# Performance work log

Hardware: AMD Instinct MI355X
Metric: run time of the kernel (lower is better)

## Reference

```python
import jax, jax.numpy as jnp
import numpy as np

N_HEADS = 6
HEAD_SIZE = 64


def setup_inputs() -> dict:
    key = jax.random.key(0)
    k1, k2, k3, k4 = jax.random.split(key, 4)
    B, T, C = 8, 2048, N_HEADS * HEAD_SIZE
    x = jax.random.normal(k1, (B, T, C), dtype=jnp.float32)
    # small init scale keeps softmax logits in a sane range
    w_qkv = jax.random.normal(k2, (C, 3 * C), dtype=jnp.float32) * 0.05
    w_proj = jax.random.normal(k3, (C, C), dtype=jnp.float32) * 0.05
    b_proj = jax.random.normal(k4, (C,), dtype=jnp.float32) * 0.05
    return {"x": x, "w_qkv": w_qkv, "w_proj": w_proj, "b_proj": b_proj}


def reference(x, w_qkv, w_proj, b_proj):
    B, T, C = x.shape
    qkv = x @ w_qkv                      # [B, T, 3C]
    q, k, v = jnp.split(qkv, 3, axis=2)
    # [B, T, C] -> [B, H, T, D]
    def heads(t):
        return t.reshape(B, T, N_HEADS, HEAD_SIZE).transpose(0, 2, 1, 3)
    q, k, v = heads(q), heads(k), heads(v)
    scale = HEAD_SIZE ** -0.5
    scores = jnp.einsum('bhqd,bhkd->bhqk', q, k) * scale   # [B, H, T, T]
    causal = jnp.tril(jnp.ones((T, T), dtype=bool))
    scores = jnp.where(causal[None, None], scores, jnp.float32(-jnp.inf))
    weights = jax.nn.softmax(scores, axis=-1)
    # dropout is identity in eval mode
    out = jnp.einsum('bhqk,bhkd->bhqd', weights, v)          # [B, H, T, D]
    out = out.transpose(0, 2, 1, 3).reshape(B, T, C)
    return out @ w_proj + b_proj
```

## Files before the change

kernel.cpp:

```cpp
#include <hip/hip_runtime.h>
#include <hip/hip_bf16.h>

typedef __bf16 bf16_t;
typedef __bf16 bf16x8 __attribute__((ext_vector_type(8)));
typedef __bf16 bf16x4 __attribute__((ext_vector_type(4)));
typedef float floatx4 __attribute__((ext_vector_type(4)));
typedef unsigned uint32x2 __attribute__((ext_vector_type(2)));

#define MFMA16(a, b, c) __builtin_amdgcn_mfma_f32_16x16x32_bf16(a, b, c, 0, 0, 0)

#if __has_builtin(__builtin_amdgcn_exp2f)
#define EXP2F(x) __builtin_amdgcn_exp2f(x)
#else
#define EXP2F(x) __expf((x)*0.693147180559945f)
#endif

__device__ __forceinline__ void async_copy16(const bf16_t* g, bf16_t* l) {
    __builtin_amdgcn_global_load_lds((const __attribute__((address_space(1))) void*)g,
                                     (__attribute__((address_space(3))) void*)l, 16, 0, 0);
}

__device__ __forceinline__ unsigned cvt_pk_bf16(float lo, float hi) {
    unsigned r;
    asm("v_cvt_pk_bf16_f32 %0, %1, %2" : "=v"(r) : "v"(lo), "v"(hi));
    return r;
}

__device__ __forceinline__ void plane32(unsigned& x, unsigned& y) {
#if __has_builtin(__builtin_amdgcn_permlane32_swap)
    uint32x2 r = __builtin_amdgcn_permlane32_swap(x, y, false, false);
    x = r[0]; y = r[1];
#else
    asm("v_permlane32_swap_b32 %0, %1" : "+v"(x), "+v"(y));
#endif
}
__device__ __forceinline__ void plane16(unsigned& x, unsigned& y) {
#if __has_builtin(__builtin_amdgcn_permlane16_swap)
    uint32x2 r = __builtin_amdgcn_permlane16_swap(x, y, false, false);
    x = r[0]; y = r[1];
#else
    asm("v_permlane16_swap_b32 %0, %1" : "+v"(x), "+v"(y));
#endif
}

__device__ __forceinline__ bf16x8 pack_pfrag(const floatx4& sE, const floatx4& sO) {
    unsigned a0 = cvt_pk_bf16(sE[0], sE[1]);
    unsigned a1 = cvt_pk_bf16(sE[2], sE[3]);
    unsigned b0 = cvt_pk_bf16(sO[0], sO[1]);
    unsigned b1 = cvt_pk_bf16(sO[2], sO[3]);
    plane32(a0, b0);
    plane32(a1, b1);
    plane16(a0, b0);
    plane16(a1, b1);
    union { unsigned u[4]; bf16x8 v; } r;
    r.u[0] = a0; r.u[1] = a1; r.u[2] = b0; r.u[3] = b1;
    return r.v;
}

__global__ void prep_fused(const float* __restrict__ x, const float* __restrict__ w_qkv,
                           const float* __restrict__ w_proj, bf16_t* __restrict__ xb,
                           bf16_t* __restrict__ wqkvT, bf16_t* __restrict__ wprojT) {
    const int bx = blockIdx.x, tid = threadIdx.x;
    if (bx < 3072) {
        size_t i = ((size_t)bx * 256 + tid) * 8;
        float4 v0 = *(const float4*)(x + i);
        float4 v1 = *(const float4*)(x + i + 4);
        bf16x8 o = {(bf16_t)v0.x, (bf16_t)v0.y, (bf16_t)v0.z, (bf16_t)v0.w,
                    (bf16_t)v1.x, (bf16_t)v1.y, (bf16_t)v1.z, (bf16_t)v1.w};
        *(bf16x8*)(xb + i) = o;
        return;
    }
    __shared__ float tile[32][33];
    int which, n0, k0, Nd;
    if (bx < 3072 + 432) {
        int idx = bx - 3072;
        which = 0; Nd = 1152; n0 = (idx % 36) * 32; k0 = (idx / 36) * 32;
    } else {
        int idx = bx - 3072 - 432;
        which = 1; Nd = 384; n0 = (idx % 12) * 32; k0 = (idx / 12) * 32;
    }
    const float* in = which ? w_proj : w_qkv;
    bf16_t* out = which ? wprojT : wqkvT;
    const int tx = tid & 31, ty = tid >> 5;
#pragma unroll
    for (int i = 0; i < 4; i++)
        tile[ty + i * 8][tx] = in[(size_t)(k0 + ty + i * 8) * Nd + n0 + tx];
    __syncthreads();
#pragma unroll
    for (int i = 0; i < 4; i++) {
        int n = n0 + ty + i * 8;
        float v = tile[tx][ty + i * 8];
        if (!which && n < 384) v *= 0.1803368851f;
        out[(size_t)n * 384 + k0 + tx] = (bf16_t)v;
    }
}

__global__ __launch_bounds__(256, 3)
void gemm_qkv(const bf16_t* __restrict__ A, const bf16_t* __restrict__ Bt,
              bf16_t* __restrict__ qkv, bf16_t* __restrict__ Vt, int M, int N, int K) {
    __shared__ __align__(16) bf16_t As[2][128 * 32];
    __shared__ __align__(16) bf16_t Bs[2][128 * 32];
    const int nblk = blockIdx.x;
    const int wgl = ((nblk & 7) * 144) + (nblk >> 3);
    const int row0 = (wgl / 9) * 128, col0 = (wgl % 9) * 128;
    const int tid = threadIdx.x;
    const int wave = tid >> 6, lane = tid & 63;
    const int wm = wave >> 1, wn = wave & 1;
    const int quad = lane >> 4, l16 = lane & 15;
    const int swz = l16 & 3;

    floatx4 acc[4][4];
#pragma unroll
    for (int i = 0; i < 4; i++)
#pragma unroll
        for (int j = 0; j < 4; j++) acc[i][j] = (floatx4){0.f, 0.f, 0.f, 0.f};

    auto stage = [&](int buf, int k0) {
#pragma unroll
        for (int it = 0; it < 2; it++) {
            int cb = wave * 64 + it * 256;
            int c = cb + lane;
            int r = c >> 2;
            int col = k0 + (((c & 3) ^ (r & 3)) * 8);
            async_copy16(A + (size_t)(row0 + r) * K + col, &As[buf][0] + cb * 8);
            async_copy16(Bt + (size_t)(col0 + r) * K + col, &Bs[buf][0] + cb * 8);
        }
    };

    const int nk = K >> 5;
    stage(0, 0);
    for (int kt = 0; kt < nk; kt++) {
        __syncthreads();
        if (kt + 1 < nk) stage((kt + 1) & 1, (kt + 1) * 32);
        const bf16_t* as = &As[kt & 1][0];
        const bf16_t* bs = &Bs[kt & 1][0];
        bf16x8 af[4], bfr[4];
#pragma unroll
        for (int i = 0; i < 4; i++)
            af[i] = *(const bf16x8*)(as + (wm * 64 + i * 16 + l16) * 32 + ((quad ^ swz) * 8));
#pragma unroll
        for (int j = 0; j < 4; j++)
            bfr[j] = *(const bf16x8*)(bs + (wn * 64 + j * 16 + l16) * 32 + ((quad ^ swz) * 8));
#pragma unroll
        for (int i = 0; i < 4; i++)
#pragma unroll
            for (int j = 0; j < 4; j++) acc[i][j] = MFMA16(bfr[j], af[i], acc[i][j]);
    }
    if (col0 < 768) {
#pragma unroll
        for (int i = 0; i < 4; i++) {
            const size_t row = (size_t)(row0 + wm * 64 + i * 16 + l16);
#pragma unroll
            for (int j = 0; j < 4; j++) {
                const int colb = col0 + wn * 64 + j * 16 + quad * 4;
                bf16x4 v = {(bf16_t)acc[i][j][0], (bf16_t)acc[i][j][1],
                            (bf16_t)acc[i][j][2], (bf16_t)acc[i][j][3]};
                *(bf16x4*)(qkv + row * N + colb) = v;
            }
        }
    } else {
        __syncthreads();
        bf16_t* myb = &As[0][0] + wave * 4096;
#pragma unroll
        for (int i = 0; i < 4; i++)
#pragma unroll
            for (int j = 0; j < 4; j++)
#pragma unroll
                for (int r = 0; r < 4; r++) {
                    int d2 = j * 16 + quad * 4 + r;
                    int t2 = i * 16 + l16;
                    myb[d2 * 64 + (((t2 >> 3) ^ (d2 & 7)) * 8) + (t2 & 7)] =
                        (bf16_t)acc[i][j][r];
                }
        asm volatile("s_waitcnt lgkmcnt(0)" ::: "memory");
        const int row_t = row0 + wm * 64;
        const int b = row_t >> 11;
        const int tt = (row_t & 2047) >> 6;
        const int h = (col0 - 768 + wn * 64) >> 6;
        bf16_t* vout = Vt + (((size_t)(b * 6 + h) * 32 + tt) << 12);
#pragma unroll
        for (int it = 0; it < 8; it++) {
            int d2 = it * 8 + (lane >> 3);
            int cl = lane & 7;
            bf16x8 v = *(const bf16x8*)(myb + d2 * 64 + ((cl ^ (d2 & 7)) * 8));
            *(bf16x8*)(vout + d2 * 64 + cl * 8) = v;
        }
    }
}

__global__ __launch_bounds__(256, 3)
void gemm_out(const bf16_t* __restrict__ A, const bf16_t* __restrict__ Bt,
              float* __restrict__ C, int M, int N, int K, const float* __restrict__ bias) {
    __shared__ __align__(16) bf16_t As[2][64 * 32];
    __shared__ __align__(16) bf16_t Bs[2][128 * 32];
    const int nblk = blockIdx.x;
    const int wgl = ((nblk & 7) * 96) + (nblk >> 3);
    const int row0 = (wgl / 3) * 64, col0 = (wgl % 3) * 128;
    const int tid = threadIdx.x;
    const int wave = tid >> 6, lane = tid & 63;
    const int wm = wave >> 1, wn = wave & 1;
    const int quad = lane >> 4, l16 = lane & 15;
    const int swz = l16 & 3;

    floatx4 acc[2][4];
#pragma unroll
    for (int i = 0; i < 2; i++)
#pragma unroll
        for (int j = 0; j < 4; j++) acc[i][j] = (floatx4){0.f, 0.f, 0.f, 0.f};

    auto stage = [&](int buf, int k0) {
        {
            int c = wave * 64 + lane;
            int r = c >> 2;
            int col = k0 + (((c & 3) ^ (r & 3)) * 8);
            async_copy16(A + (size_t)(row0 + r) * K + col, &As[buf][0] + (wave * 64) * 8);
        }
#pragma unroll
        for (int it = 0; it < 2; it++) {
            int cb = wave * 64 + it * 256;
            int c = cb + lane;
            int r = c >> 2;
            int col = k0 + (((c & 3) ^ (r & 3)) * 8);
            async_copy16(Bt + (size_t)(col0 + r) * K + col, &Bs[buf][0] + cb * 8);
        }
    };

    const int nk = K >> 5;
    stage(0, 0);
    for (int kt = 0; kt < nk; kt++) {
        __syncthreads();
        if (kt + 1 < nk) stage((kt + 1) & 1, (kt + 1) * 32);
        const bf16_t* as = &As[kt & 1][0];
        const bf16_t* bs = &Bs[kt & 1][0];
        bf16x8 af[2], bfr[4];
#pragma unroll
        for (int i = 0; i < 2; i++)
            af[i] = *(const bf16x8*)(as + (wm * 32 + i * 16 + l16) * 32 + ((quad ^ swz) * 8));
#pragma unroll
        for (int j = 0; j < 4; j++)
            bfr[j] = *(const bf16x8*)(bs + (wn * 64 + j * 16 + l16) * 32 + ((quad ^ swz) * 8));
#pragma unroll
        for (int i = 0; i < 2; i++)
#pragma unroll
            for (int j = 0; j < 4; j++) acc[i][j] = MFMA16(bfr[j], af[i], acc[i][j]);
    }
#pragma unroll
    for (int i = 0; i < 2; i++) {
        const size_t row = (size_t)(row0 + wm * 32 + i * 16 + l16);
#pragma unroll
        for (int j = 0; j < 4; j++) {
            const int colb = col0 + wn * 64 + j * 16 + quad * 4;
            float4 bv = *(const float4*)(bias + colb);
            float4 v = {acc[i][j][0] + bv.x, acc[i][j][1] + bv.y,
                        acc[i][j][2] + bv.z, acc[i][j][3] + bv.w};
            *(float4*)(C + row * N + colb) = v;
        }
    }
}

__device__ __forceinline__ void stage64(const bf16_t* __restrict__ gtile, int stride,
                                        bf16_t* lds, int wave, int lane) {
#pragma unroll
    for (int it = 0; it < 2; it++) {
        int cb = wave * 64 + it * 256;
        int c = cb + lane;
        int r = c >> 3;
        int col = ((c & 7) ^ (r & 7)) * 8;
        async_copy16(gtile + (size_t)r * stride + col, lds + cb * 8);
    }
}

__global__ __launch_bounds__(256, 4)
void attn_kernel(const bf16_t* __restrict__ qkv, const bf16_t* __restrict__ Vt,
                 bf16_t* __restrict__ attn_out, float* __restrict__ Opart,
                 float* __restrict__ Lpart) {
    constexpr int T = 2048, C3 = 1152;
    const int n = blockIdx.x;
    const int xcd = n & 7, i = n >> 3;
    const int j = i / 6, gl = i % 6;
    const int g = xcd * 6 + gl;
    const int h = g % 6, b = g / 6;
    const bool isD = (0x6AD5AB50u >> j) & 1;
    const int c = (int)((j < 16 ? (0x98A7B6CD5E4F3210ull >> (4 * j))
                                : (0xF01E2D3C45B6A798ull >> (4 * (j - 16)))) & 15);
    const int qa = c, qb = 31 - c;
    const int kt0 = isD ? 0 : (c + 1);
    const int kt1 = isD ? qa : qb;
    const int tid = threadIdx.x;
    const int wave = tid >> 6, lane = tid & 63;
    const int quad = lane >> 4, l16 = lane & 15;

    __shared__ __align__(16) bf16_t Ks[2][64 * 64];
    __shared__ __align__(16) bf16_t Vs[2][64 * 64];

    const bf16_t* kbase = qkv + (size_t)b * T * C3 + 384 + h * 64;
    const bf16_t* vbase = Vt + (((size_t)(b * 6 + h) * 32) << 12);

    const bf16_t* qpb =
        qkv + ((size_t)b * T + qb * 64 + wave * 16 + l16) * C3 + h * 64 + quad * 8;
    bf16x8 qB0 = *(const bf16x8*)qpb, qB1 = *(const bf16x8*)(qpb + 32);
    bf16x8 qA0, qA1;
    if (isD) {
        const bf16_t* qpa =
            qkv + ((size_t)b * T + qa * 64 + wave * 16 + l16) * C3 + h * 64 + quad * 8;
        qA0 = *(const bf16x8*)qpa; qA1 = *(const bf16x8*)(qpa + 32);
    }

    floatx4 oA[4], oB[4];
    float lpA = 0.f, lpB = 0.f;
#pragma unroll
    for (int r = 0; r < 4; r++) {
        oA[r] = (floatx4){0.f, 0.f, 0.f, 0.f};
        oB[r] = (floatx4){0.f, 0.f, 0.f, 0.f};
    }
    const floatx4 C0 = {-13.f, -13.f, -13.f, -13.f};

    stage64(kbase + (size_t)kt0 * 64 * C3, C3, &Ks[kt0 & 1][0], wave, lane);
    stage64(vbase + ((size_t)kt0 << 12), 64, &Vs[kt0 & 1][0], wave, lane);

    const int swz = l16 & 7;

    for (int kt = kt0; kt <= kt1; kt++) {
        __syncthreads();
        if (kt < kt1) {
            stage64(kbase + (size_t)(kt + 1) * 64 * C3, C3, &Ks[(kt + 1) & 1][0], wave, lane);
            stage64(vbase + ((size_t)(kt + 1) << 12), 64, &Vs[(kt + 1) & 1][0], wave, lane);
        }
        const bf16_t* kb = &Ks[kt & 1][0];
        const bf16_t* vb = &Vs[kt & 1][0];
        const bool doA = isD;

        floatx4 sA[4], sB[4];
        __builtin_amdgcn_s_setprio(1);
#pragma unroll
        for (int nt = 0; nt < 4; nt++) {
            bf16x8 kf0 = *(const bf16x8*)(kb + (nt * 16 + l16) * 64 + ((quad ^ swz) * 8));
            bf16x8 kf1 = *(const bf16x8*)(kb + (nt * 16 + l16) * 64 + (((4 + quad) ^ swz) * 8));
            sB[nt] = MFMA16(kf0, qB0, C0);
            sB[nt] = MFMA16(kf1, qB1, sB[nt]);
            if (doA) {
                sA[nt] = MFMA16(kf0, qA0, C0);
                sA[nt] = MFMA16(kf1, qA1, sA[nt]);
            }
        }
        __builtin_amdgcn_s_setprio(0);

        if (kt == qb) {
#pragma unroll
            for (int nt = 0; nt < 4; nt++)
#pragma unroll
                for (int r = 0; r < 4; r++)
                    if (nt * 16 + quad * 4 + r > wave * 16 + l16) sB[nt][r] = -1e30f;
        }
        if (doA && kt == qa) {
#pragma unroll
            for (int nt = 0; nt < 4; nt++)
#pragma unroll
                for (int r = 0; r < 4; r++)
                    if (nt * 16 + quad * 4 + r > wave * 16 + l16) sA[nt][r] = -1e30f;
        }

        bf16x8 pB0, pB1, pA0, pA1;
#pragma unroll
        for (int hf = 0; hf < 2; hf++) {
#pragma unroll
            for (int nt = hf * 2; nt < hf * 2 + 2; nt++)
#pragma unroll
                for (int r = 0; r < 4; r++) {
                    float p = EXP2F(sB[nt][r]);
                    sB[nt][r] = p;
                    lpB += p;
                }
            if (hf == 0) pB0 = pack_pfrag(sB[0], sB[1]);
            else         pB1 = pack_pfrag(sB[2], sB[3]);
        }
        if (doA) {
#pragma unroll
            for (int hf = 0; hf < 2; hf++) {
#pragma unroll
                for (int nt = hf * 2; nt < hf * 2 + 2; nt++)
#pragma unroll
                    for (int r = 0; r < 4; r++) {
                        float p = EXP2F(sA[nt][r]);
                        sA[nt][r] = p;
                        lpA += p;
                    }
                if (hf == 0) pA0 = pack_pfrag(sA[0], sA[1]);
                else         pA1 = pack_pfrag(sA[2], sA[3]);
            }
        }

        __builtin_amdgcn_s_setprio(1);
#pragma unroll
        for (int dt = 0; dt < 4; dt++) {
            bf16x8 vf0 = *(const bf16x8*)(vb + (dt * 16 + l16) * 64 + ((quad ^ swz) * 8));
            bf16x8 vf1 = *(const bf16x8*)(vb + (dt * 16 + l16) * 64 + (((4 + quad) ^ swz) * 8));
            oB[dt] = MFMA16(vf0, pB0, oB[dt]);
            oB[dt] = MFMA16(vf1, pB1, oB[dt]);
            if (doA) {
                oA[dt] = MFMA16(vf0, pA0, oA[dt]);
                oA[dt] = MFMA16(vf1, pA1, oA[dt]);
            }
        }
        __builtin_amdgcn_s_setprio(0);
    }

    lpB += __shfl_xor(lpB, 16); lpB += __shfl_xor(lpB, 32);

    if (isD) {
        lpA += __shfl_xor(lpA, 16); lpA += __shfl_xor(lpA, 32);
        const float invA = 1.0f / lpA;
        const int tA = qa * 64 + wave * 16 + l16;
#pragma unroll
        for (int dt = 0; dt < 4; dt++) {
            bf16x4 va = {(bf16_t)(oA[dt][0] * invA), (bf16_t)(oA[dt][1] * invA),
                         (bf16_t)(oA[dt][2] * invA), (bf16_t)(oA[dt][3] * invA)};
            int col = h * 64 + dt * 16 + quad * 4;
            *(bf16x4*)(attn_out + ((size_t)b * T + tA) * 384 + col) = va;
        }
    }

    const int slot = isD ? 0 : 1;
    const size_t tile_id = ((size_t)g * 16 + (qb - 16)) * 2 + slot;
    const size_t pb = (tile_id * 64 + (wave * 16 + l16)) * 64;
#pragma unroll
    for (int dt = 0; dt < 4; dt++) {
        float4 v = {oB[dt][0], oB[dt][1], oB[dt][2], oB[dt][3]};
        *(float4*)(Opart + pb + dt * 16 + quad * 4) = v;
    }
    if (quad == 0) Lpart[tile_id * 64 + wave * 16 + l16] = lpB;
}

__global__ __launch_bounds__(256)
void attn_norm(const float* __restrict__ Opart, const float* __restrict__ Lpart,
               bf16_t* __restrict__ attn_out) {
    constexpr int T = 2048;
    const int n = blockIdx.x;
    const int xcd = n & 7, i = n >> 3;
    const int gl = i % 6, tq = i / 6;
    const int g = xcd * 6 + gl;
    const int h = g % 6, b = g / 6;
    const int tid = threadIdx.x;
    const int r = tid >> 2, d0 = (tid & 3) * 16;
    const size_t t2 = ((size_t)g * 16 + tq) * 2;
    const float lp = Lpart[t2 * 64 + r] + Lpart[(t2 + 1) * 64 + r];
    const float inv = 1.0f / lp;
    const size_t b0 = ((t2 + 0) * 64 + r) * 64 + d0;
    const size_t b1 = ((t2 + 1) * 64 + r) * 64 + d0;
    bf16_t ov[16];
#pragma unroll
    for (int cchunk = 0; cchunk < 4; cchunk++) {
        float4 x0 = *(const float4*)(Opart + b0 + cchunk * 4);
        float4 x1 = *(const float4*)(Opart + b1 + cchunk * 4);
        ov[cchunk * 4 + 0] = (bf16_t)((x0.x + x1.x) * inv);
        ov[cchunk * 4 + 1] = (bf16_t)((x0.y + x1.y) * inv);
        ov[cchunk * 4 + 2] = (bf16_t)((x0.z + x1.z) * inv);
        ov[cchunk * 4 + 3] = (bf16_t)((x0.w + x1.w) * inv);
    }
    bf16_t* dst = attn_out + ((size_t)b * T + 1024 + tq * 64 + r) * 384 + h * 64 + d0;
    *(bf16x8*)(dst) = *(bf16x8*)(ov);
    *(bf16x8*)(dst + 8) = *(bf16x8*)(ov + 8);
}

extern "C" void kernel_launch(void* const* d_in, const int* in_sizes, int n_in,
                              void* d_out, int out_size, void* d_ws, size_t ws_size,
                              hipStream_t stream) {
    const float* x      = (const float*)d_in[0];
    const float* w_qkv  = (const float*)d_in[1];
    const float* w_proj = (const float*)d_in[2];
    const float* b_proj = (const float*)d_in[3];
    float* out = (float*)d_out;

    bf16_t* ws = (bf16_t*)d_ws;
    bf16_t* wqkvT = ws;
    bf16_t* wprojT = wqkvT + 1152 * 384;
    bf16_t* xb = wprojT + 384 * 384;
    bf16_t* qkv = xb + (size_t)16384 * 384;
    bf16_t* Vt = qkv + (size_t)16384 * 1152;
    bf16_t* attn = Vt + (size_t)48 * 64 * 2048;
    float* Opart = (float*)(attn + (size_t)16384 * 384);
    float* Lpart = Opart + (size_t)48 * 16 * 2 * 64 * 64;

    hipLaunchKernelGGL(prep_fused, dim3(3072 + 432 + 144), dim3(256), 0, stream,
                       x, w_qkv, w_proj, xb, wqkvT, wprojT);
    hipLaunchKernelGGL(gemm_qkv, dim3(1152), dim3(256), 0, stream,
                       xb, wqkvT, qkv, Vt, 16384, 1152, 384);
    hipLaunchKernelGGL(attn_kernel, dim3(1536), dim3(256), 0, stream,
                       qkv, Vt, attn, Opart, Lpart);
    hipLaunchKernelGGL(attn_norm, dim3(768), dim3(256), 0, stream, Opart, Lpart, attn);
    hipLaunchKernelGGL(gemm_out, dim3(768), dim3(256), 0, stream,
                       attn, wprojT, out, 16384, 384, 384, b_proj);
}
```

Measured before the change: 175.6 us.

## Fuse split-tile reduction into attention kernel and compute row sums via MFMA

Removes the separate attn_norm kernel. The two blocks sharing a query tile now coordinate with an atomic ticket: the first writes its partial O and row sums, and the second spins on a ready flag, then combines, normalizes and writes bf16 output. Row sums of P are computed with an MFMA against a ones vector instead of scalar adds plus cross-lane shuffles. This saves a launch and a round trip through Opart, but adds a memset, atomics and a spin-wait that could stall if the first block's partner is not resident.

```diff
diff --git a/kernel.cpp b/kernel.cpp
--- a/kernel.cpp
+++ b/kernel.cpp
@@ -273,7 +273,8 @@
 __global__ __launch_bounds__(256, 4)
 void attn_kernel(const bf16_t* __restrict__ qkv, const bf16_t* __restrict__ Vt,
                  bf16_t* __restrict__ attn_out, float* __restrict__ Opart,
-                 float* __restrict__ Lpart) {
+                 float* __restrict__ Lpart, unsigned* __restrict__ cnt,
+                 unsigned* __restrict__ rdy) {
     constexpr int T = 2048, C3 = 1152;
     const int n = blockIdx.x;
     const int xcd = n & 7, i = n >> 3;
@@ -307,13 +308,15 @@
     }
 
     floatx4 oA[4], oB[4];
-    float lpA = 0.f, lpB = 0.f;
+    floatx4 lpA4 = (floatx4){0.f, 0.f, 0.f, 0.f}, lpB4 = (floatx4){0.f, 0.f, 0.f, 0.f};
 #pragma unroll
     for (int r = 0; r < 4; r++) {
         oA[r] = (floatx4){0.f, 0.f, 0.f, 0.f};
         oB[r] = (floatx4){0.f, 0.f, 0.f, 0.f};
     }
     const floatx4 C0 = {-13.f, -13.f, -13.f, -13.f};
+    const bf16_t one1 = (bf16_t)1.f;
+    const bf16x8 onesv = {one1, one1, one1, one1, one1, one1, one1, one1};
 
     stage64(kbase + (size_t)kt0 * 64 * C3, C3, &Ks[kt0 & 1][0], wave, lane);
     stage64(vbase + ((size_t)kt0 << 12), 64, &Vs[kt0 & 1][0], wave, lane);
@@ -366,11 +369,7 @@
 #pragma unroll
             for (int nt = hf * 2; nt < hf * 2 + 2; nt++)
 #pragma unroll
-                for (int r = 0; r < 4; r++) {
-                    float p = EXP2F(sB[nt][r]);
-                    sB[nt][r] = p;
-                    lpB += p;
-                }
+                for (int r = 0; r < 4; r++) sB[nt][r] = EXP2F(sB[nt][r]);
             if (hf == 0) pB0 = pack_pfrag(sB[0], sB[1]);
             else         pB1 = pack_pfrag(sB[2], sB[3]);
         }
@@ -380,17 +379,19 @@
 #pragma unroll
                 for (int nt = hf * 2; nt < hf * 2 + 2; nt++)
 #pragma unroll
-                    for (int r = 0; r < 4; r++) {
-                        float p = EXP2F(sA[nt][r]);
-                        sA[nt][r] = p;
-                        lpA += p;
-                    }
+                    for (int r = 0; r < 4; r++) sA[nt][r] = EXP2F(sA[nt][r]);
                 if (hf == 0) pA0 = pack_pfrag(sA[0], sA[1]);
                 else         pA1 = pack_pfrag(sA[2], sA[3]);
             }
         }
 
         __builtin_amdgcn_s_setprio(1);
+        lpB4 = MFMA16(onesv, pB0, lpB4);
+        lpB4 = MFMA16(onesv, pB1, lpB4);
+        if (doA) {
+            lpA4 = MFMA16(onesv, pA0, lpA4);
+            lpA4 = MFMA16(onesv, pA1, lpA4);
+        }
 #pragma unroll
         for (int dt = 0; dt < 4; dt++) {
             bf16x8 vf0 = *(const bf16x8*)(vb + (dt * 16 + l16) * 64 + ((quad ^ swz) * 8));
@@ -405,12 +406,11 @@
         __builtin_amdgcn_s_setprio(0);
     }
 
-    lpB += __shfl_xor(lpB, 16); lpB += __shfl_xor(lpB, 32);
+    const int row = wave * 16 + l16;
 
     if (isD) {
-        lpA += __shfl_xor(lpA, 16); lpA += __shfl_xor(lpA, 32);
-        const float invA = 1.0f / lpA;
-        const int tA = qa * 64 + wave * 16 + l16;
+        const float invA = 1.0f / lpA4[0];
+        const int tA = qa * 64 + row;
 #pragma unroll
         for (int dt = 0; dt < 4; dt++) {
             bf16x4 va = {(bf16_t)(oA[dt][0] * invA), (bf16_t)(oA[dt][1] * invA),
@@ -420,46 +420,43 @@
         }
     }
 
-    const int slot = isD ? 0 : 1;
-    const size_t tile_id = ((size_t)g * 16 + (qb - 16)) * 2 + slot;
-    const size_t pb = (tile_id * 64 + (wave * 16 + l16)) * 64;
-#pragma unroll
-    for (int dt = 0; dt < 4; dt++) {
-        float4 v = {oB[dt][0], oB[dt][1], oB[dt][2], oB[dt][3]};
-        *(float4*)(Opart + pb + dt * 16 + quad * 4) = v;
-    }
-    if (quad == 0) Lpart[tile_id * 64 + wave * 16 + l16] = lpB;
-}
-
-__global__ __launch_bounds__(256)
-void attn_norm(const float* __restrict__ Opart, const float* __restrict__ Lpart,
-               bf16_t* __restrict__ attn_out) {
-    constexpr int T = 2048;
-    const int n = blockIdx.x;
-    const int xcd = n & 7, i = n >> 3;
-    const int gl = i % 6, tq = i / 6;
-    const int g = xcd * 6 + gl;
-    const int h = g % 6, b = g / 6;
-    const int tid = threadIdx.x;
-    const int r = tid >> 2, d0 = (tid & 3) * 16;
-    const size_t t2 = ((size_t)g * 16 + tq) * 2;
-    const float lp = Lpart[t2 * 64 + r] + Lpart[(t2 + 1) * 64 + r];
-    const float inv = 1.0f / lp;
-    const size_t b0 = ((t2 + 0) * 64 + r) * 64 + d0;
-    const size_t b1 = ((t2 + 1) * 64 + r) * 64 + d0;
-    bf16_t ov[16];
-#pragma unroll
-    for (int cchunk = 0; cchunk < 4; cchunk++) {
-        float4 x0 = *(const float4*)(Opart + b0 + cchunk * 4);
-        float4 x1 = *(const float4*)(Opart + b1 + cchunk * 4);
-        ov[cchunk * 4 + 0] = (bf16_t)((x0.x + x1.x) * inv);
-        ov[cchunk * 4 + 1] = (bf16_t)((x0.y + x1.y) * inv);
-        ov[cchunk * 4 + 2] = (bf16_t)((x0.z + x1.z) * inv);
-        ov[cchunk * 4 + 3] = (bf16_t)((x0.w + x1.w) * inv);
-    }
-    bf16_t* dst = attn_out + ((size_t)b * T + 1024 + tq * 64 + r) * 384 + h * 64 + d0;
-    *(bf16x8*)(dst) = *(bf16x8*)(ov);
-    *(bf16x8*)(dst + 8) = *(bf16x8*)(ov + 8);
+    const float lpB = lpB4[0];
+    const int tile = g * 16 + (qb - 16);
+    __shared__ unsigned s_tk;
+    if (tid == 0) s_tk = atomicAdd(&cnt[tile], 1u);
+    __syncthreads();
+    const size_t pb = ((size_t)tile * 64 + row) * 64;
+    if (s_tk == 0) {
+#pragma unroll
+        for (int dt = 0; dt < 4; dt++) {
+            float4 v = {oB[dt][0], oB[dt][1], oB[dt][2], oB[dt][3]};
+            *(float4*)(Opart + pb + dt * 16 + quad * 4) = v;
+        }
+        if (quad == 0) Lpart[tile * 64 + row] = lpB;
+        __syncthreads();
+        if (tid == 0) {
+            __threadfence();
+            __hip_atomic_store(&rdy[tile], 1u, __ATOMIC_RELEASE, __HIP_MEMORY_SCOPE_AGENT);
+        }
+    } else {
+        if (tid == 0) {
+            while (__hip_atomic_load(&rdy[tile], __ATOMIC_ACQUIRE,
+                                     __HIP_MEMORY_SCOPE_AGENT) == 0u)
+                __builtin_amdgcn_s_sleep(8);
+        }
+        __syncthreads();
+        const float lp = lpB + Lpart[tile * 64 + row];
+        const float inv = 1.0f / lp;
+        const int tB = qb * 64 + row;
+#pragma unroll
+        for (int dt = 0; dt < 4; dt++) {
+            float4 p0 = *(const float4*)(Opart + pb + dt * 16 + quad * 4);
+            bf16x4 v = {(bf16_t)((oB[dt][0] + p0.x) * inv), (bf16_t)((oB[dt][1] + p0.y) * inv),
+                        (bf16_t)((oB[dt][2] + p0.z) * inv), (bf16_t)((oB[dt][3] + p0.w) * inv)};
+            int col = h * 64 + dt * 16 + quad * 4;
+            *(bf16x4*)(attn_out + ((size_t)b * T + tB) * 384 + col) = v;
+        }
+    }
 }
 
 extern "C" void kernel_launch(void* const* d_in, const int* in_sizes, int n_in,
@@ -479,15 +476,16 @@
     bf16_t* Vt = qkv + (size_t)16384 * 1152;
     bf16_t* attn = Vt + (size_t)48 * 64 * 2048;
     float* Opart = (float*)(attn + (size_t)16384 * 384);
-    float* Lpart = Opart + (size_t)48 * 16 * 2 * 64 * 64;
-
+    float* Lpart = Opart + (size_t)768 * 64 * 64;
+    unsigned* flags = (unsigned*)(Lpart + 768 * 64);
+
+    hipMemsetAsync(flags, 0, 1536 * sizeof(unsigned), stream);
     hipLaunchKernelGGL(prep_fused, dim3(3072 + 432 + 144), dim3(256), 0, stream,
                        x, w_qkv, w_proj, xb, wqkvT, wprojT);
     hipLaunchKernelGGL(gemm_qkv, dim3(1152), dim3(256), 0, stream,
                        xb, wqkvT, qkv, Vt, 16384, 1152, 384);
     hipLaunchKernelGGL(attn_kernel, dim3(1536), dim3(256), 0, stream,
-                       qkv, Vt, attn, Opart, Lpart);
-    hipLaunchKernelGGL(attn_norm, dim3(768), dim3(256), 0, stream, Opart, Lpart, attn);
+                       qkv, Vt, attn, Opart, Lpart, flags, flags + 768);
     hipLaunchKernelGGL(gemm_out, dim3(768), dim3(256), 0, stream,
                        attn, wprojT, out, 16384, 384, 384, b_proj);
 }
```

Measured after the change: 223.6 us. 1.27x slower.
